# Performance work log

Measured on AMD Instinct MI355X. Metric: run time of the kernel, lower is better.

Reference implementation:

```python
import jax, jax.numpy as jnp
import numpy as np

D_MODEL = 1024
D_STATE = 16
D_CONV = 4
EXPAND = 2
D_INNER = EXPAND * D_MODEL
DT_RANK = -(-D_MODEL // 16)  # ceil(d_model/16) = 64
LN_EPS = 1e-5


def setup_inputs() -> dict:
    key = jax.random.key(0)
    ks = jax.random.split(key, 10)
    b, l = 1, 2048
    s = 0.02
    x = jax.random.normal(ks[0], (b, l, D_MODEL), dtype=jnp.float32)
    gamma = jnp.ones((D_MODEL,), jnp.float32)
    beta = jnp.zeros((D_MODEL,), jnp.float32)
    w_in = jax.random.normal(ks[1], (2 * D_INNER, D_MODEL), jnp.float32) * s
    conv_w = jax.random.normal(ks[2], (D_INNER, D_CONV), jnp.float32) * s
    conv_b = jnp.zeros((D_INNER,), jnp.float32)
    w_x = jax.random.normal(ks[3], (DT_RANK + 2 * D_STATE, D_INNER), jnp.float32) * s
    w_dt = jax.random.normal(ks[4], (D_INNER, DT_RANK), jnp.float32) * s
    b_dt = jax.random.normal(ks[5], (D_INNER,), jnp.float32) * s
    A_log = jnp.log(jnp.broadcast_to(jnp.arange(1, D_STATE + 1, dtype=jnp.float32)[None, :], (D_INNER, D_STATE)))
    Dp = jnp.ones((D_INNER,), jnp.float32)
    w_out = jax.random.normal(ks[6], (D_MODEL, D_INNER), jnp.float32) * s
    return {"x": x, "gamma": gamma, "beta": beta, "w_in": w_in, "conv_w": conv_w,
            "conv_b": conv_b, "w_x": w_x, "w_dt": w_dt, "b_dt": b_dt,
            "A_log": A_log, "Dp": Dp, "w_out": w_out}


def _combine(e1, e2):
    # (a2, b2) o (a1, b1) = (a2*a1, a2*b1 + b2); e2 is the later element
    a1, b1 = e1
    a2, b2 = e2
    return (a2 * a1, a2 * b1 + b2)


def _forward(x, gamma, beta, w_in, conv_w, conv_b, w_x, w_dt, b_dt, A_log, Dp, w_out):
    residual = x
    # LayerNorm
    mu = jnp.mean(x, axis=-1, keepdims=True)
    var = jnp.var(x, axis=-1, keepdims=True)
    xn = (x - mu) * jax.lax.rsqrt(var + LN_EPS) * gamma + beta
    # in_proj and split
    xz = jnp.einsum('bld,ed->ble', xn, w_in)
    x_part, z = xz[..., :D_INNER], xz[..., D_INNER:]
    # causal depthwise conv1d (torch pads k-1 both sides then trims to l == left pad)
    lhs = jnp.transpose(x_part, (0, 2, 1))  # (b, d_inner, l)
    rhs = conv_w[:, None, :]                # (d_inner, 1, k)
    conv = jax.lax.conv_general_dilated(
        lhs, rhs, window_strides=(1,), padding=[(D_CONV - 1, 0)],
        dimension_numbers=('NCH', 'OIH', 'NCH'), feature_group_count=D_INNER)
    x_part = jnp.transpose(conv, (0, 2, 1)) + conv_b  # (b, l, d_inner)
    x_part = jax.nn.silu(x_part)  # dropout is identity in eval mode
    # SSM
    A = -jnp.exp(A_log)  # (d_inner, n)
    x_dbl = jnp.einsum('bld,ed->ble', x_part, w_x)
    dt = x_dbl[..., :DT_RANK]
    B = x_dbl[..., DT_RANK:DT_RANK + D_STATE]
    C = x_dbl[..., DT_RANK + D_STATE:]
    delta = jax.nn.softplus(jnp.einsum('blr,dr->bld', dt, w_dt) + b_dt)  # (b,l,d_inner)
    deltaA = jnp.exp(delta[..., None] * A[None, None])                    # (b,l,d_inner,n)
    dBu = delta[..., None] * B[:, :, None, :] * x_part[..., None]         # (b,l,d_inner,n)
    _, h = jax.lax.associative_scan(_combine, (deltaA, dBu), axis=1)
    y = jnp.sum(h * C[:, :, None, :], axis=-1) + x_part * Dp             # (b,l,d_inner)
    y = y * jax.nn.silu(z)
    out = jnp.einsum('ble,de->bld', y, w_out) + residual
    return out


def reference(x, gamma, beta, w_in, conv_w, conv_b, w_x, w_dt, b_dt, A_log, Dp, w_out):
    return _forward(x, gamma, beta, w_in, conv_w, conv_b, w_x, w_dt, b_dt, A_log, Dp, w_out)
```

## Files before the change

kernel.cpp:

```cpp
#include <hip/hip_runtime.h>
#include <math.h>

#define L_SEQ 2048
#define DM 1024
#define DI 2048
#define DS 16
#define DR 64
#define XDN 96
#define NCHUNK 64
#define TCH 32
#define KSLICES 8
#define KSL (DI / KSLICES)

typedef __attribute__((ext_vector_type(8))) short bf16x8;
typedef __attribute__((ext_vector_type(4))) float f32x4;
typedef unsigned short ushort_t;
typedef __attribute__((address_space(1))) const unsigned int GU32;
typedef __attribute__((address_space(3))) unsigned int LU32;

__device__ inline unsigned short f2bf(float f) {
  unsigned int u = __builtin_bit_cast(unsigned int, f);
  u += 0x7fffu + ((u >> 16) & 1u);
  return (unsigned short)(u >> 16);
}
__device__ inline float bf2f(unsigned short u) {
  return __builtin_bit_cast(float, (unsigned int)u << 16);
}

__device__ inline void cvt4(const float* src, ushort_t* dst, int j) {
  float4 v = ((const float4*)src)[j];
  ushort4 o;
  o.x = f2bf(v.x); o.y = f2bf(v.y); o.z = f2bf(v.z); o.w = f2bf(v.w);
  ((ushort4*)dst)[j] = o;
}

__global__ void cvt_all_kernel(const float* __restrict__ w_in,
                               const float* __restrict__ w_out,
                               const float* __restrict__ w_x,
                               const float* __restrict__ w_dt,
                               ushort_t* __restrict__ w_inb,
                               ushort_t* __restrict__ w_outb,
                               ushort_t* __restrict__ w_xb,
                               ushort_t* __restrict__ w_dtb) {
  int i = blockIdx.x * 256 + threadIdx.x;
  const int N0 = 2 * DI * DM / 4;
  const int N1 = N0 + DM * DI / 4;
  const int N2 = N1 + 128 * DI / 4;
  const int N3 = N2 + DI * DR / 4;
  if (i < N0) {
    cvt4(w_in, w_inb, i);
  } else if (i < N1) {
    cvt4(w_out, w_outb, i - N0);
  } else if (i < N2) {
    int j = i - N1;
    int e0 = j << 2;
    int row = e0 >> 11;
    int col = e0 & (DI - 1);
    ushort4 o = {0, 0, 0, 0};
    if (row < XDN) {
      float4 v = *(const float4*)(w_x + (size_t)row * DI + col);
      o.x = f2bf(v.x); o.y = f2bf(v.y); o.z = f2bf(v.z); o.w = f2bf(v.w);
    }
    ((ushort4*)w_xb)[j] = o;
  } else if (i < N3) {
    cvt4(w_dt, w_dtb, i - N2);
  }
}

__global__ void ln_kernel(const float* __restrict__ x,
                          const float* __restrict__ gamma,
                          const float* __restrict__ beta,
                          ushort_t* __restrict__ xnb) {
  int row = blockIdx.x;
  int t = threadIdx.x;
  const float4* xr = (const float4*)(x + (size_t)row * DM);
  float4 v = xr[t];
  float s = v.x + v.y + v.z + v.w;
  float s2 = v.x * v.x + v.y * v.y + v.z * v.z + v.w * v.w;
#pragma unroll
  for (int off = 32; off > 0; off >>= 1) {
    s += __shfl_down(s, off);
    s2 += __shfl_down(s2, off);
  }
  __shared__ float ls[4], ls2[4];
  if ((t & 63) == 0) { ls[t >> 6] = s; ls2[t >> 6] = s2; }
  __syncthreads();
  float tot = ls[0] + ls[1] + ls[2] + ls[3];
  float tot2 = ls2[0] + ls2[1] + ls2[2] + ls2[3];
  float mu = tot * (1.0f / DM);
  float var = tot2 * (1.0f / DM) - mu * mu;
  float r = rsqrtf(var + 1e-5f);
  float4 g = ((const float4*)gamma)[t];
  float4 b = ((const float4*)beta)[t];
  ushort4 o;
  o.x = f2bf((v.x - mu) * r * g.x + b.x);
  o.y = f2bf((v.y - mu) * r * g.y + b.y);
  o.z = f2bf((v.z - mu) * r * g.z + b.z);
  o.w = f2bf((v.w - mu) * r * g.w + b.w);
  ((ushort4*)(xnb + (size_t)row * DM))[t] = o;
}

template <int EPI>
__global__ __launch_bounds__(256) void mgemm(
    const ushort_t* __restrict__ A, int lda,
    const ushort_t* __restrict__ B, int ldb,
    void* __restrict__ Cp, int ldc, int K,
    const float* __restrict__ extra, int lde) {
  __shared__ ushort_t As[128 * 32];
  __shared__ ushort_t Bs[128 * 32];
  const int tid = threadIdx.x;
  const int lane = tid & 63;
  const int wave = tid >> 6;
  const int m0 = blockIdx.y * 128;
  const int n0 = blockIdx.x * 128;
  const int wr = (wave >> 1) * 64;
  const int wc = (wave & 1) * 64;
  const int kq = lane >> 4;
  const int rr = lane & 15;
  f32x4 acc[4][4];
#pragma unroll
  for (int i = 0; i < 4; ++i)
#pragma unroll
    for (int j = 0; j < 4; ++j) acc[i][j] = (f32x4){0.f, 0.f, 0.f, 0.f};

  const int u0 = tid, u1 = tid + 256;
  const int rA0 = u0 >> 2, cA0 = (u0 & 3) << 3;
  const int rA1 = u1 >> 2, cA1 = (u1 & 3) << 3;

  for (int k0 = 0; k0 < K; k0 += 32) {
    __syncthreads();
    __builtin_amdgcn_global_load_lds(
        (GU32*)(A + (size_t)(m0 + rA0) * lda + k0 + cA0),
        (LU32*)(As + u0 * 8), 16, 0, 0);
    __builtin_amdgcn_global_load_lds(
        (GU32*)(A + (size_t)(m0 + rA1) * lda + k0 + cA1),
        (LU32*)(As + u1 * 8), 16, 0, 0);
    __builtin_amdgcn_global_load_lds(
        (GU32*)(B + (size_t)(n0 + rA0) * ldb + k0 + cA0),
        (LU32*)(Bs + u0 * 8), 16, 0, 0);
    __builtin_amdgcn_global_load_lds(
        (GU32*)(B + (size_t)(n0 + rA1) * ldb + k0 + cA1),
        (LU32*)(Bs + u1 * 8), 16, 0, 0);
    __syncthreads();
    bf16x8 a[4], b[4];
#pragma unroll
    for (int i = 0; i < 4; ++i)
      a[i] = *(const bf16x8*)(As + (wr + i * 16 + rr) * 32 + kq * 8);
#pragma unroll
    for (int j = 0; j < 4; ++j)
      b[j] = *(const bf16x8*)(Bs + (wc + j * 16 + rr) * 32 + kq * 8);
#pragma unroll
    for (int i = 0; i < 4; ++i)
#pragma unroll
      for (int j = 0; j < 4; ++j)
        acc[i][j] = __builtin_amdgcn_mfma_f32_16x16x32_bf16(a[i], b[j], acc[i][j], 0, 0, 0);
  }
#pragma unroll
  for (int i = 0; i < 4; ++i) {
#pragma unroll
    for (int j = 0; j < 4; ++j) {
#pragma unroll
      for (int r = 0; r < 4; ++r) {
        int row = m0 + wr + i * 16 + kq * 4 + r;
        int col = n0 + wc + j * 16 + rr;
        float v = acc[i][j][r];
        if (EPI == 2) {
          v += extra[(size_t)row * lde + col];
          ((float*)Cp)[(size_t)row * ldc + col] = v;
        } else if (EPI == 4) {
          ((ushort_t*)Cp)[(size_t)row * ldc + col] = f2bf(v);
        } else if (EPI == 5) {
          v += extra[col];
          v = (v > 20.f) ? v : __logf(1.f + __expf(v));
          ((ushort_t*)Cp)[(size_t)row * ldc + col] = f2bf(v);
        } else {
          ((float*)Cp)[(size_t)row * ldc + col] = v;
        }
      }
    }
  }
}

__global__ __launch_bounds__(256) void mgemm_sk(
    const ushort_t* __restrict__ A, int lda,
    const ushort_t* __restrict__ B, int ldb,
    float* __restrict__ part) {
  __shared__ ushort_t As[128 * 32];
  __shared__ ushort_t Bs[128 * 32];
  const int tid = threadIdx.x;
  const int lane = tid & 63;
  const int wave = tid >> 6;
  const int m0 = blockIdx.y * 128;
  const int s = blockIdx.z;
  const int kbase = s * KSL;
  const int wr = (wave >> 1) * 64;
  const int wc = (wave & 1) * 64;
  const int kq = lane >> 4;
  const int rr = lane & 15;
  f32x4 acc[4][4];
#pragma unroll
  for (int i = 0; i < 4; ++i)
#pragma unroll
    for (int j = 0; j < 4; ++j) acc[i][j] = (f32x4){0.f, 0.f, 0.f, 0.f};

  const int u0 = tid, u1 = tid + 256;
  const int rA0 = u0 >> 2, cA0 = (u0 & 3) << 3;
  const int rA1 = u1 >> 2, cA1 = (u1 & 3) << 3;

  for (int k0 = 0; k0 < KSL; k0 += 32) {
    __syncthreads();
    __builtin_amdgcn_global_load_lds(
        (GU32*)(A + (size_t)(m0 + rA0) * lda + kbase + k0 + cA0),
        (LU32*)(As + u0 * 8), 16, 0, 0);
    __builtin_amdgcn_global_load_lds(
        (GU32*)(A + (size_t)(m0 + rA1) * lda + kbase + k0 + cA1),
        (LU32*)(As + u1 * 8), 16, 0, 0);
    __builtin_amdgcn_global_load_lds(
        (GU32*)(B + (size_t)rA0 * ldb + kbase + k0 + cA0),
        (LU32*)(Bs + u0 * 8), 16, 0, 0);
    __builtin_amdgcn_global_load_lds(
        (GU32*)(B + (size_t)rA1 * ldb + kbase + k0 + cA1),
        (LU32*)(Bs + u1 * 8), 16, 0, 0);
    __syncthreads();
    bf16x8 a[4], b[4];
#pragma unroll
    for (int i = 0; i < 4; ++i)
      a[i] = *(const bf16x8*)(As + (wr + i * 16 + rr) * 32 + kq * 8);
#pragma unroll
    for (int j = 0; j < 4; ++j)
      b[j] = *(const bf16x8*)(Bs + (wc + j * 16 + rr) * 32 + kq * 8);
#pragma unroll
    for (int i = 0; i < 4; ++i)
#pragma unroll
      for (int j = 0; j < 4; ++j)
        acc[i][j] = __builtin_amdgcn_mfma_f32_16x16x32_bf16(a[i], b[j], acc[i][j], 0, 0, 0);
  }
#pragma unroll
  for (int i = 0; i < 4; ++i)
#pragma unroll
    for (int j = 0; j < 4; ++j)
#pragma unroll
      for (int r = 0; r < 4; ++r) {
        int row = m0 + wr + i * 16 + kq * 4 + r;
        int col = wc + j * 16 + rr;
        part[((size_t)s * L_SEQ + row) * 128 + col] = acc[i][j][r];
      }
}

__global__ void reduce_xdbl_kernel(const float* __restrict__ part,
                                   float* __restrict__ xdbl,
                                   ushort_t* __restrict__ dtb) {
  int i = blockIdx.x * 256 + threadIdx.x;
  int col = i & 127;
  int row = i >> 7;
  float s = 0.f;
#pragma unroll
  for (int k = 0; k < KSLICES; ++k) s += part[(size_t)k * (L_SEQ * 128) + i];
  if (col < DR) dtb[(size_t)row * DR + col] = f2bf(s);
  if (col < XDN) xdbl[(size_t)row * XDN + col] = s;
}

__global__ void conv_silu_kernel(const ushort_t* __restrict__ xzb,
                                 const float* __restrict__ conv_w,
                                 const float* __restrict__ conv_b,
                                 ushort_t* __restrict__ xconvb) {
  int i = blockIdx.x * blockDim.x + threadIdx.x;
  int d0 = (i & (DI / 4 - 1)) << 2;
  int t = i >> 9;
  float4 bia = *(const float4*)(conv_b + d0);
  float acc[4] = {bia.x, bia.y, bia.z, bia.w};
  float w[4][4];
#pragma unroll
  for (int c = 0; c < 4; ++c) {
    float4 wv = *(const float4*)(conv_w + (size_t)(d0 + c) * 4);
    w[c][0] = wv.x; w[c][1] = wv.y; w[c][2] = wv.z; w[c][3] = wv.w;
  }
#pragma unroll
  for (int j = 0; j < 4; ++j) {
    int tt = t - 3 + j;
    if (tt >= 0) {
      ushort4 xv = *(const ushort4*)(xzb + (size_t)tt * (2 * DI) + d0);
      acc[0] += bf2f(xv.x) * w[0][j];
      acc[1] += bf2f(xv.y) * w[1][j];
      acc[2] += bf2f(xv.z) * w[2][j];
      acc[3] += bf2f(xv.w) * w[3][j];
    }
  }
  ushort4 o;
  o.x = f2bf(acc[0] / (1.f + __expf(-acc[0])));
  o.y = f2bf(acc[1] / (1.f + __expf(-acc[1])));
  o.z = f2bf(acc[2] / (1.f + __expf(-acc[2])));
  o.w = f2bf(acc[3] / (1.f + __expf(-acc[3])));
  *(ushort4*)(xconvb + (size_t)t * DI + d0) = o;
}

__global__ void scan_chunk_kernel(const ushort_t* __restrict__ deltab,
                                  const ushort_t* __restrict__ ub,
                                  const float* __restrict__ xdbl,
                                  const float* __restrict__ A_log,
                                  float* __restrict__ P,
                                  float* __restrict__ HB) {
  int d = blockIdx.x * blockDim.x + threadIdx.x;
  int c = blockIdx.y;
  int t0 = c * TCH;
  float Aval[DS];
#pragma unroll
  for (int q = 0; q < 4; ++q) {
    float4 al = *(const float4*)(A_log + (size_t)d * DS + q * 4);
    Aval[q * 4 + 0] = -__expf(al.x);
    Aval[q * 4 + 1] = -__expf(al.y);
    Aval[q * 4 + 2] = -__expf(al.z);
    Aval[q * 4 + 3] = -__expf(al.w);
  }
  float h[DS], p[DS];
#pragma unroll
  for (int n = 0; n < DS; ++n) { h[n] = 0.f; p[n] = 1.f; }
  for (int t = t0; t < t0 + TCH; ++t) {
    float dlt = bf2f(deltab[(size_t)t * DI + d]);
    float uv = bf2f(ub[(size_t)t * DI + d]);
    float du = dlt * uv;
    float Bv[DS];
#pragma unroll
    for (int q = 0; q < 4; ++q) {
      float4 b4 = *(const float4*)(xdbl + (size_t)t * XDN + DR + q * 4);
      Bv[q * 4 + 0] = b4.x; Bv[q * 4 + 1] = b4.y;
      Bv[q * 4 + 2] = b4.z; Bv[q * 4 + 3] = b4.w;
    }
#pragma unroll
    for (int n = 0; n < DS; ++n) {
      float dA = __expf(dlt * Aval[n]);
      p[n] *= dA;
      h[n] = dA * h[n] + du * Bv[n];
    }
  }
#pragma unroll
  for (int n = 0; n < DS; ++n) {
    size_t idx = ((size_t)c * DS + n) * DI + d;
    P[idx] = p[n];
    HB[idx] = h[n];
  }
}

__global__ void scan_prop_kernel(const float* __restrict__ P,
                                 const float* __restrict__ HB,
                                 float* __restrict__ HIN) {
  int dn = blockIdx.x * blockDim.x + threadIdx.x;
  float h = 0.f;
#pragma unroll 4
  for (int c = 0; c < NCHUNK; ++c) {
    size_t idx = (size_t)c * (DI * DS) + dn;
    HIN[idx] = h;
    h = P[idx] * h + HB[idx];
  }
}

__global__ void scan_final_kernel(const ushort_t* __restrict__ deltab,
                                  const ushort_t* __restrict__ ub,
                                  const float* __restrict__ xdbl,
                                  const ushort_t* __restrict__ xzb,
                                  const float* __restrict__ A_log,
                                  const float* __restrict__ Dp,
                                  const float* __restrict__ HIN,
                                  ushort_t* __restrict__ ygb) {
  int d = blockIdx.x * blockDim.x + threadIdx.x;
  int c = blockIdx.y;
  int t0 = c * TCH;
  float Aval[DS];
#pragma unroll
  for (int q = 0; q < 4; ++q) {
    float4 al = *(const float4*)(A_log + (size_t)d * DS + q * 4);
    Aval[q * 4 + 0] = -__expf(al.x);
    Aval[q * 4 + 1] = -__expf(al.y);
    Aval[q * 4 + 2] = -__expf(al.z);
    Aval[q * 4 + 3] = -__expf(al.w);
  }
  float Dval = Dp[d];
  float h[DS];
#pragma unroll
  for (int n = 0; n < DS; ++n) h[n] = HIN[((size_t)c * DS + n) * DI + d];
  for (int t = t0; t < t0 + TCH; ++t) {
    float dlt = bf2f(deltab[(size_t)t * DI + d]);
    float uv = bf2f(ub[(size_t)t * DI + d]);
    float du = dlt * uv;
    float Bv[DS], Cv[DS];
#pragma unroll
    for (int q = 0; q < 4; ++q) {
      float4 b4 = *(const float4*)(xdbl + (size_t)t * XDN + DR + q * 4);
      float4 c4 = *(const float4*)(xdbl + (size_t)t * XDN + DR + DS + q * 4);
      Bv[q * 4 + 0] = b4.x; Bv[q * 4 + 1] = b4.y;
      Bv[q * 4 + 2] = b4.z; Bv[q * 4 + 3] = b4.w;
      Cv[q * 4 + 0] = c4.x; Cv[q * 4 + 1] = c4.y;
      Cv[q * 4 + 2] = c4.z; Cv[q * 4 + 3] = c4.w;
    }
    float acc = uv * Dval;
#pragma unroll
    for (int n = 0; n < DS; ++n) {
      float dA = __expf(dlt * Aval[n]);
      h[n] = dA * h[n] + du * Bv[n];
      acc += h[n] * Cv[n];
    }
    float z = bf2f(xzb[(size_t)t * (2 * DI) + DI + d]);
    float sz = z / (1.f + __expf(-z));
    ygb[(size_t)t * DI + d] = f2bf(acc * sz);
  }
}

extern "C" void kernel_launch(void* const* d_in, const int* in_sizes, int n_in,
                              void* d_out, int out_size, void* d_ws, size_t ws_size,
                              hipStream_t stream) {
  const float* x = (const float*)d_in[0];
  const float* gamma = (const float*)d_in[1];
  const float* beta = (const float*)d_in[2];
  const float* w_in = (const float*)d_in[3];
  const float* conv_w = (const float*)d_in[4];
  const float* conv_b = (const float*)d_in[5];
  const float* w_x = (const float*)d_in[6];
  const float* w_dt = (const float*)d_in[7];
  const float* b_dt = (const float*)d_in[8];
  const float* A_log = (const float*)d_in[9];
  const float* Dp = (const float*)d_in[10];
  const float* w_out = (const float*)d_in[11];
  float* out = (float*)d_out;

  float* ws = (float*)d_ws;
  float* xdbl = ws;
  float* P = xdbl + (size_t)L_SEQ * XDN;
  float* HB = P + (size_t)NCHUNK * DI * DS;
  float* HIN = HB + (size_t)NCHUNK * DI * DS;
  float* part = HIN + (size_t)NCHUNK * DI * DS;
  ushort_t* xzb = (ushort_t*)(part + (size_t)KSLICES * L_SEQ * 128);
  ushort_t* xconvb = xzb + (size_t)L_SEQ * 2 * DI;
  ushort_t* deltab = xconvb + (size_t)L_SEQ * DI;
  ushort_t* ygb = deltab + (size_t)L_SEQ * DI;
  ushort_t* xnb = ygb + (size_t)L_SEQ * DI;
  ushort_t* w_inb = xnb + (size_t)L_SEQ * DM;
  ushort_t* w_outb = w_inb + (size_t)(2 * DI) * DM;
  ushort_t* w_xb = w_outb + (size_t)DM * DI;
  ushort_t* w_dtb = w_xb + (size_t)128 * DI;
  ushort_t* dtb = w_dtb + (size_t)DI * DR;

  {
    int units = (2 * DI * DM + DM * DI + 128 * DI + DI * DR) / 4;
    cvt_all_kernel<<<(units + 255) / 256, 256, 0, stream>>>(
        w_in, w_out, w_x, w_dt, w_inb, w_outb, w_xb, w_dtb);
  }
  ln_kernel<<<L_SEQ, 256, 0, stream>>>(x, gamma, beta, xnb);
  mgemm<4><<<dim3((2 * DI) / 128, L_SEQ / 128), 256, 0, stream>>>(
      xnb, DM, w_inb, DM, xzb, 2 * DI, DM, nullptr, 0);
  conv_silu_kernel<<<(L_SEQ * DI / 4) / 256, 256, 0, stream>>>(
      xzb, conv_w, conv_b, xconvb);
  mgemm_sk<<<dim3(1, L_SEQ / 128, KSLICES), 256, 0, stream>>>(
      xconvb, DI, w_xb, DI, part);
  reduce_xdbl_kernel<<<(L_SEQ * 128) / 256, 256, 0, stream>>>(part, xdbl, dtb);
  mgemm<5><<<dim3(DI / 128, L_SEQ / 128), 256, 0, stream>>>(
      dtb, DR, w_dtb, DR, deltab, DI, DR, b_dt, 0);
  scan_chunk_kernel<<<dim3(DI / 256, NCHUNK), 256, 0, stream>>>(
      deltab, xconvb, xdbl, A_log, P, HB);
  scan_prop_kernel<<<(DI * DS) / 256, 256, 0, stream>>>(P, HB, HIN);
  scan_final_kernel<<<dim3(DI / 256, NCHUNK), 256, 0, stream>>>(
      deltab, xconvb, xdbl, xzb, A_log, Dp, HIN, ygb);
  mgemm<2><<<dim3(DM / 128, L_SEQ / 128), 256, 0, stream>>>(
      ygb, DI, w_outb, DI, out, DM, DI, x, DM);
}
```

Baseline: 180.3 us.

## Use K=64 tiles with XOR-swizzled LDS and split-K for out_proj

The GEMM kernel now stages 64-wide K tiles in LDS with an XOR swizzle, so there are fewer barriers per K step and fewer LDS bank conflicts. The separate split-K kernel is folded into the generic mgemm through blockIdx.z and a new partial-output epilogue. The out_proj GEMM is split into two K halves to launch more blocks, and a new reduce kernel sums the halves and adds the residual. This costs an extra pass over the partials, and the partials reuse the xzb buffer after the scan has consumed it.

```diff
diff --git a/kernel.cpp b/kernel.cpp
--- a/kernel.cpp
+++ b/kernel.cpp
@@ -104,15 +104,16 @@
 __global__ __launch_bounds__(256) void mgemm(
     const ushort_t* __restrict__ A, int lda,
     const ushort_t* __restrict__ B, int ldb,
-    void* __restrict__ Cp, int ldc, int K,
-    const float* __restrict__ extra, int lde) {
-  __shared__ ushort_t As[128 * 32];
-  __shared__ ushort_t Bs[128 * 32];
+    void* __restrict__ Cp, int ldc, int ksl,
+    const float* __restrict__ extra) {
+  __shared__ ushort_t As[128 * 64];
+  __shared__ ushort_t Bs[128 * 64];
   const int tid = threadIdx.x;
   const int lane = tid & 63;
   const int wave = tid >> 6;
   const int m0 = blockIdx.y * 128;
   const int n0 = blockIdx.x * 128;
+  const int kbase = blockIdx.z * ksl;
   const int wr = (wave >> 1) * 64;
   const int wc = (wave & 1) * 64;
   const int kq = lane >> 4;
@@ -123,37 +124,49 @@
 #pragma unroll
     for (int j = 0; j < 4; ++j) acc[i][j] = (f32x4){0.f, 0.f, 0.f, 0.f};
 
-  const int u0 = tid, u1 = tid + 256;
-  const int rA0 = u0 >> 2, cA0 = (u0 & 3) << 3;
-  const int rA1 = u1 >> 2, cA1 = (u1 & 3) << 3;
-
-  for (int k0 = 0; k0 < K; k0 += 32) {
+  int ur[4], uc[4];
+#pragma unroll
+  for (int q = 0; q < 4; ++q) {
+    int u = tid + 256 * q;
+    ur[q] = u >> 3;
+    uc[q] = (((u & 7) ^ (ur[q] & 7)) << 3);
+  }
+
+  for (int k0 = kbase; k0 < kbase + ksl; k0 += 64) {
     __syncthreads();
-    __builtin_amdgcn_global_load_lds(
-        (GU32*)(A + (size_t)(m0 + rA0) * lda + k0 + cA0),
-        (LU32*)(As + u0 * 8), 16, 0, 0);
-    __builtin_amdgcn_global_load_lds(
-        (GU32*)(A + (size_t)(m0 + rA1) * lda + k0 + cA1),
-        (LU32*)(As + u1 * 8), 16, 0, 0);
-    __builtin_amdgcn_global_load_lds(
-        (GU32*)(B + (size_t)(n0 + rA0) * ldb + k0 + cA0),
-        (LU32*)(Bs + u0 * 8), 16, 0, 0);
-    __builtin_amdgcn_global_load_lds(
-        (GU32*)(B + (size_t)(n0 + rA1) * ldb + k0 + cA1),
-        (LU32*)(Bs + u1 * 8), 16, 0, 0);
+#pragma unroll
+    for (int q = 0; q < 4; ++q)
+      __builtin_amdgcn_global_load_lds(
+          (GU32*)(A + (size_t)(m0 + ur[q]) * lda + k0 + uc[q]),
+          (LU32*)(As + (tid + 256 * q) * 8), 16, 0, 0);
+#pragma unroll
+    for (int q = 0; q < 4; ++q)
+      __builtin_amdgcn_global_load_lds(
+          (GU32*)(B + (size_t)(n0 + ur[q]) * ldb + k0 + uc[q]),
+          (LU32*)(Bs + (tid + 256 * q) * 8), 16, 0, 0);
     __syncthreads();
-    bf16x8 a[4], b[4];
-#pragma unroll
-    for (int i = 0; i < 4; ++i)
-      a[i] = *(const bf16x8*)(As + (wr + i * 16 + rr) * 32 + kq * 8);
-#pragma unroll
-    for (int j = 0; j < 4; ++j)
-      b[j] = *(const bf16x8*)(Bs + (wc + j * 16 + rr) * 32 + kq * 8);
-#pragma unroll
-    for (int i = 0; i < 4; ++i)
-#pragma unroll
-      for (int j = 0; j < 4; ++j)
-        acc[i][j] = __builtin_amdgcn_mfma_f32_16x16x32_bf16(a[i], b[j], acc[i][j], 0, 0, 0);
+#pragma unroll
+    for (int kk = 0; kk < 2; ++kk) {
+      const int sw = ((rr & 7) << 4);
+      bf16x8 a[4], b[4];
+#pragma unroll
+      for (int i = 0; i < 4; ++i) {
+        int row = wr + i * 16 + rr;
+        int off = ((kk * 64 + kq * 16) ^ sw);
+        a[i] = *(const bf16x8*)((const char*)As + row * 128 + off);
+      }
+#pragma unroll
+      for (int j = 0; j < 4; ++j) {
+        int row = wc + j * 16 + rr;
+        int off = ((kk * 64 + kq * 16) ^ sw);
+        b[j] = *(const bf16x8*)((const char*)Bs + row * 128 + off);
+      }
+#pragma unroll
+      for (int i = 0; i < 4; ++i)
+#pragma unroll
+        for (int j = 0; j < 4; ++j)
+          acc[i][j] = __builtin_amdgcn_mfma_f32_16x16x32_bf16(a[i], b[j], acc[i][j], 0, 0, 0);
+    }
   }
 #pragma unroll
   for (int i = 0; i < 4; ++i) {
@@ -164,87 +177,18 @@
         int row = m0 + wr + i * 16 + kq * 4 + r;
         int col = n0 + wc + j * 16 + rr;
         float v = acc[i][j][r];
-        if (EPI == 2) {
-          v += extra[(size_t)row * lde + col];
-          ((float*)Cp)[(size_t)row * ldc + col] = v;
-        } else if (EPI == 4) {
+        if (EPI == 4) {
           ((ushort_t*)Cp)[(size_t)row * ldc + col] = f2bf(v);
         } else if (EPI == 5) {
           v += extra[col];
           v = (v > 20.f) ? v : __logf(1.f + __expf(v));
           ((ushort_t*)Cp)[(size_t)row * ldc + col] = f2bf(v);
-        } else {
-          ((float*)Cp)[(size_t)row * ldc + col] = v;
+        } else if (EPI == 6) {
+          ((float*)Cp)[((size_t)blockIdx.z * L_SEQ + row) * ldc + col] = v;
         }
       }
     }
   }
-}
-
-__global__ __launch_bounds__(256) void mgemm_sk(
-    const ushort_t* __restrict__ A, int lda,
-    const ushort_t* __restrict__ B, int ldb,
-    float* __restrict__ part) {
-  __shared__ ushort_t As[128 * 32];
-  __shared__ ushort_t Bs[128 * 32];
-  const int tid = threadIdx.x;
-  const int lane = tid & 63;
-  const int wave = tid >> 6;
-  const int m0 = blockIdx.y * 128;
-  const int s = blockIdx.z;
-  const int kbase = s * KSL;
-  const int wr = (wave >> 1) * 64;
-  const int wc = (wave & 1) * 64;
-  const int kq = lane >> 4;
-  const int rr = lane & 15;
-  f32x4 acc[4][4];
-#pragma unroll
-  for (int i = 0; i < 4; ++i)
-#pragma unroll
-    for (int j = 0; j < 4; ++j) acc[i][j] = (f32x4){0.f, 0.f, 0.f, 0.f};
-
-  const int u0 = tid, u1 = tid + 256;
-  const int rA0 = u0 >> 2, cA0 = (u0 & 3) << 3;
-  const int rA1 = u1 >> 2, cA1 = (u1 & 3) << 3;
-
-  for (int k0 = 0; k0 < KSL; k0 += 32) {
-    __syncthreads();
-    __builtin_amdgcn_global_load_lds(
-        (GU32*)(A + (size_t)(m0 + rA0) * lda + kbase + k0 + cA0),
-        (LU32*)(As + u0 * 8), 16, 0, 0);
-    __builtin_amdgcn_global_load_lds(
-        (GU32*)(A + (size_t)(m0 + rA1) * lda + kbase + k0 + cA1),
-        (LU32*)(As + u1 * 8), 16, 0, 0);
-    __builtin_amdgcn_global_load_lds(
-        (GU32*)(B + (size_t)rA0 * ldb + kbase + k0 + cA0),
-        (LU32*)(Bs + u0 * 8), 16, 0, 0);
-    __builtin_amdgcn_global_load_lds(
-        (GU32*)(B + (size_t)rA1 * ldb + kbase + k0 + cA1),
-        (LU32*)(Bs + u1 * 8), 16, 0, 0);
-    __syncthreads();
-    bf16x8 a[4], b[4];
-#pragma unroll
-    for (int i = 0; i < 4; ++i)
-      a[i] = *(const bf16x8*)(As + (wr + i * 16 + rr) * 32 + kq * 8);
-#pragma unroll
-    for (int j = 0; j < 4; ++j)
-      b[j] = *(const bf16x8*)(Bs + (wc + j * 16 + rr) * 32 + kq * 8);
-#pragma unroll
-    for (int i = 0; i < 4; ++i)
-#pragma unroll
-      for (int j = 0; j < 4; ++j)
-        acc[i][j] = __builtin_amdgcn_mfma_f32_16x16x32_bf16(a[i], b[j], acc[i][j], 0, 0, 0);
-  }
-#pragma unroll
-  for (int i = 0; i < 4; ++i)
-#pragma unroll
-    for (int j = 0; j < 4; ++j)
-#pragma unroll
-      for (int r = 0; r < 4; ++r) {
-        int row = m0 + wr + i * 16 + kq * 4 + r;
-        int col = wc + j * 16 + rr;
-        part[((size_t)s * L_SEQ + row) * 128 + col] = acc[i][j][r];
-      }
 }
 
 __global__ void reduce_xdbl_kernel(const float* __restrict__ part,
@@ -258,6 +202,21 @@
   for (int k = 0; k < KSLICES; ++k) s += part[(size_t)k * (L_SEQ * 128) + i];
   if (col < DR) dtb[(size_t)row * DR + col] = f2bf(s);
   if (col < XDN) xdbl[(size_t)row * XDN + col] = s;
+}
+
+__global__ void reduce_out_kernel(const float* __restrict__ part,
+                                  const float* __restrict__ x,
+                                  float* __restrict__ out) {
+  int i = blockIdx.x * 256 + threadIdx.x;
+  float4 p0 = ((const float4*)part)[i];
+  float4 p1 = ((const float4*)(part + (size_t)L_SEQ * DM))[i];
+  float4 xr = ((const float4*)x)[i];
+  float4 o;
+  o.x = p0.x + p1.x + xr.x;
+  o.y = p0.y + p1.y + xr.y;
+  o.z = p0.z + p1.z + xr.z;
+  o.w = p0.w + p1.w + xr.w;
+  ((float4*)out)[i] = o;
 }
 
 __global__ void conv_silu_kernel(const ushort_t* __restrict__ xzb,
@@ -438,6 +397,7 @@
   ushort_t* w_xb = w_outb + (size_t)DM * DI;
   ushort_t* w_dtb = w_xb + (size_t)128 * DI;
   ushort_t* dtb = w_dtb + (size_t)DI * DR;
+  float* part_out = (float*)xzb;
 
   {
     int units = (2 * DI * DM + DM * DI + 128 * DI + DI * DR) / 4;
@@ -445,20 +405,21 @@
         w_in, w_out, w_x, w_dt, w_inb, w_outb, w_xb, w_dtb);
   }
   ln_kernel<<<L_SEQ, 256, 0, stream>>>(x, gamma, beta, xnb);
-  mgemm<4><<<dim3((2 * DI) / 128, L_SEQ / 128), 256, 0, stream>>>(
-      xnb, DM, w_inb, DM, xzb, 2 * DI, DM, nullptr, 0);
+  mgemm<4><<<dim3((2 * DI) / 128, L_SEQ / 128, 1), 256, 0, stream>>>(
+      xnb, DM, w_inb, DM, xzb, 2 * DI, DM, nullptr);
   conv_silu_kernel<<<(L_SEQ * DI / 4) / 256, 256, 0, stream>>>(
       xzb, conv_w, conv_b, xconvb);
-  mgemm_sk<<<dim3(1, L_SEQ / 128, KSLICES), 256, 0, stream>>>(
-      xconvb, DI, w_xb, DI, part);
+  mgemm<6><<<dim3(1, L_SEQ / 128, KSLICES), 256, 0, stream>>>(
+      xconvb, DI, w_xb, DI, part, 128, KSL, nullptr);
   reduce_xdbl_kernel<<<(L_SEQ * 128) / 256, 256, 0, stream>>>(part, xdbl, dtb);
-  mgemm<5><<<dim3(DI / 128, L_SEQ / 128), 256, 0, stream>>>(
-      dtb, DR, w_dtb, DR, deltab, DI, DR, b_dt, 0);
+  mgemm<5><<<dim3(DI / 128, L_SEQ / 128, 1), 256, 0, stream>>>(
+      dtb, DR, w_dtb, DR, deltab, DI, DR, b_dt);
   scan_chunk_kernel<<<dim3(DI / 256, NCHUNK), 256, 0, stream>>>(
       deltab, xconvb, xdbl, A_log, P, HB);
   scan_prop_kernel<<<(DI * DS) / 256, 256, 0, stream>>>(P, HB, HIN);
   scan_final_kernel<<<dim3(DI / 256, NCHUNK), 256, 0, stream>>>(
       deltab, xconvb, xdbl, xzb, A_log, Dp, HIN, ygb);
-  mgemm<2><<<dim3(DM / 128, L_SEQ / 128), 256, 0, stream>>>(
-      ygb, DI, w_outb, DI, out, DM, DI, x, DM);
-}
+  mgemm<6><<<dim3(DM / 128, L_SEQ / 128, 2), 256, 0, stream>>>(
+      ygb, DI, w_outb, DI, part_out, DM, DI / 2, nullptr);
+  reduce_out_kernel<<<(L_SEQ * DM / 4) / 256, 256, 0, stream>>>(part_out, x, out);
+}
```

After: 161.3 us. -10.5%, faster.
